# Kernel tuning notes

Measured on AMD Instinct MI355X. Metric: run time of the kernel, lower is better.

The kernel has to match this reference:

```python
import jax, jax.numpy as jnp
import numpy as np
import math

NUM_HEADS = 16


def setup_inputs() -> dict:
    key = jax.random.key(0)
    ks = jax.random.split(key, 7)
    B, S, D = 2, 2048, 1024
    scale = 1.0 / math.sqrt(D)
    return {
        "query": jax.random.normal(ks[0], (B, S, D), jnp.float32),
        "key": jax.random.normal(ks[1], (B, S, D), jnp.float32),
        "value": jax.random.normal(ks[2], (B, S, D), jnp.float32),
        "Wq": jax.random.normal(ks[3], (D, D), jnp.float32) * scale,
        "Wk": jax.random.normal(ks[4], (D, D), jnp.float32) * scale,
        "Wv": jax.random.normal(ks[5], (D, D), jnp.float32) * scale,
        "Wo": jax.random.normal(ks[6], (D, D), jnp.float32) * scale,
    }


def reference(query, key, value, Wq, Wk, Wv, Wo):
    B, Sq, D = query.shape
    Sk = key.shape[1]
    H = NUM_HEADS
    dk = D // H
    # torch Linear (no bias): y = x @ W.T
    q = (query @ Wq.T).reshape(B, Sq, H, dk).transpose(0, 2, 1, 3)  # [B,H,Sq,dk]
    k = (key @ Wk.T).reshape(B, Sk, H, dk).transpose(0, 2, 1, 3)
    v = (value @ Wv.T).reshape(B, Sk, H, dk).transpose(0, 2, 1, 3)
    scores = jnp.einsum("bhqd,bhkd->bhqk", q, k) / jnp.sqrt(jnp.float32(dk))
    causal = jnp.tril(jnp.ones((Sq, Sk), dtype=bool))  # mask_future=True
    scores = jnp.where(causal[None, None], scores, jnp.float32(-1e9))
    p = jax.nn.softmax(scores, axis=-1)
    x = jnp.einsum("bhqk,bhkd->bhqd", p, v)  # [B,H,Sq,dk]
    x = x.transpose(0, 2, 1, 3).reshape(B, Sq, D)
    return x @ Wo.T
```

## Files before the change

### kernel.cpp

```cpp
#include <hip/hip_runtime.h>
#include <hip/hip_bf16.h>
#include <stdint.h>

#define D_MODEL 1024
#define NHEADS  16
#define DK      64
#define SEQ     2048
#define BATCH   2

typedef __bf16 bf16x8 __attribute__((ext_vector_type(8)));
typedef __bf16 bf16x4 __attribute__((ext_vector_type(4)));
typedef float  f32x4  __attribute__((ext_vector_type(4)));

__device__ __forceinline__ void async_copy16(const void* g, void* l) {
  __builtin_amdgcn_global_load_lds(
      (__attribute__((address_space(1))) void*)g,
      (__attribute__((address_space(3))) void*)l, 16, 0, 0);
}

__global__ void cast_all(const float* __restrict__ q, const float* __restrict__ k,
                         const float* __restrict__ v, const float* __restrict__ wq,
                         const float* __restrict__ wk, const float* __restrict__ wv,
                         const float* __restrict__ wo,
                         __bf16* __restrict__ oq, __bf16* __restrict__ ok,
                         __bf16* __restrict__ ov, __bf16* __restrict__ owq,
                         __bf16* __restrict__ owk, __bf16* __restrict__ owv,
                         __bf16* __restrict__ owo) {
  constexpr unsigned Q4 = (unsigned)(BATCH * SEQ * D_MODEL) / 4;
  constexpr unsigned W4 = (unsigned)(D_MODEL * D_MODEL) / 4;
  unsigned i = blockIdx.x * 256u + threadIdx.x;
  const float* in; __bf16* out; unsigned off;
  if (i < 3 * Q4) {
    unsigned z = i >> 20; off = i & (Q4 - 1);
    in  = z == 0 ? q : z == 1 ? k : v;
    out = z == 0 ? oq : z == 1 ? ok : ov;
  } else {
    unsigned j = i - 3 * Q4;
    unsigned z = j >> 18; off = j & (W4 - 1);
    in  = z == 0 ? wq : z == 1 ? wk : z == 2 ? wv : wo;
    out = z == 0 ? owq : z == 1 ? owk : z == 2 ? owv : owo;
  }
  float4 val = *(const float4*)(in + (size_t)off * 4);
  bf16x4 o;
  o.x = (__bf16)val.x; o.y = (__bf16)val.y; o.z = (__bf16)val.z; o.w = (__bf16)val.w;
  *(bf16x4*)(out + (size_t)off * 4) = o;
}

template <int BM, int BN, typename OutT>
__global__ __launch_bounds__(256, 2)
void gemm_bt(const __bf16* __restrict__ A0, const __bf16* __restrict__ A1, const __bf16* __restrict__ A2,
             const __bf16* __restrict__ B0, const __bf16* __restrict__ B1, const __bf16* __restrict__ B2,
             OutT* __restrict__ C0, OutT* __restrict__ C1, OutT* __restrict__ C2,
             int M, int N, int K) {
  constexpr int MI = BM / 32, NJ = BN / 32;
  const __bf16* A; const __bf16* Bm; OutT* C;
  if (blockIdx.z == 0)      { A = A0; Bm = B0; C = C0; }
  else if (blockIdx.z == 1) { A = A1; Bm = B1; C = C1; }
  else                      { A = A2; Bm = B2; C = C2; }

  __shared__ __bf16 Ash[BM * 32];
  __shared__ __bf16 Bsh[BN * 32];

  const int tid  = threadIdx.x;
  const int lane = tid & 63;
  const int w    = tid >> 6;
  const int quad = lane >> 4;
  const int l16  = lane & 15;
  const int wr   = w >> 1, wc = w & 1;
  const size_t m0 = (size_t)blockIdx.x * BM;
  const size_t n0 = (size_t)blockIdx.y * BN;

  f32x4 acc[MI][NJ] = {};

  for (int k0 = 0; k0 < K; k0 += 32) {
#pragma unroll
    for (int it = 0; it < BM / 64; ++it) {
      int slot = tid + it * 256;
      async_copy16(A + (m0 + (slot >> 2)) * K + k0 + (slot & 3) * 8, &Ash[slot * 8]);
    }
#pragma unroll
    for (int it = 0; it < BN / 64; ++it) {
      int slot = tid + it * 256;
      async_copy16(Bm + (n0 + (slot >> 2)) * K + k0 + (slot & 3) * 8, &Bsh[slot * 8]);
    }
    __syncthreads();
    bf16x8 af[MI], bfr[NJ];
#pragma unroll
    for (int i = 0; i < MI; ++i)
      af[i] = *(const bf16x8*)&Ash[(wr * (BM / 2) + i * 16 + l16) * 32 + quad * 8];
#pragma unroll
    for (int j = 0; j < NJ; ++j)
      bfr[j] = *(const bf16x8*)&Bsh[(wc * (BN / 2) + j * 16 + l16) * 32 + quad * 8];
#pragma unroll
    for (int i = 0; i < MI; ++i)
#pragma unroll
      for (int j = 0; j < NJ; ++j)
        acc[i][j] = __builtin_amdgcn_mfma_f32_16x16x32_bf16(af[i], bfr[j], acc[i][j], 0, 0, 0);
    __syncthreads();
  }

#pragma unroll
  for (int i = 0; i < MI; ++i)
#pragma unroll
    for (int j = 0; j < NJ; ++j)
#pragma unroll
      for (int r = 0; r < 4; ++r) {
        size_t row = m0 + wr * (BM / 2) + i * 16 + quad * 4 + r;
        size_t col = n0 + wc * (BN / 2) + j * 16 + l16;
        C[row * N + col] = (OutT)acc[i][j][r];
      }
}

__global__ __launch_bounds__(256, 4)
void transpose_v(const __bf16* __restrict__ Vp, __bf16* __restrict__ Vt) {
  __shared__ __bf16 L[64 * 65];
  const int t  = threadIdx.x;
  const int s0 = blockIdx.x * 64, d0 = blockIdx.y * 64, b = blockIdx.z;
#pragma unroll
  for (int it = 0; it < 2; ++it) {
    int slot = t + it * 256;
    int sl = slot >> 3, c = slot & 7;
    int4 v = *(const int4*)&Vp[((size_t)(b * SEQ + s0 + sl)) * D_MODEL + d0 + c * 8];
    __bf16 tmp[8];
    *(int4*)tmp = v;
#pragma unroll
    for (int e = 0; e < 8; ++e) L[(c * 8 + e) * 65 + sl] = tmp[e];
  }
  __syncthreads();
#pragma unroll
  for (int it = 0; it < 2; ++it) {
    int slot = t + it * 256;
    int dl = slot >> 3, c2 = slot & 7;
    __bf16 tmp[8];
#pragma unroll
    for (int e = 0; e < 8; ++e) tmp[e] = L[dl * 65 + c2 * 8 + e];
    *(int4*)&Vt[((size_t)(b * D_MODEL + d0 + dl)) * SEQ + s0 + c2 * 8] = *(int4*)tmp;
  }
}

#define PS_W 40

__global__ __launch_bounds__(256, 3)
void attn_kernel(const __bf16* __restrict__ Qp, const __bf16* __restrict__ Kp,
                 const __bf16* __restrict__ Vt, __bf16* __restrict__ Xo) {
  __shared__ __bf16 Kb[2 * 2 * 64 * 32];
  __shared__ __bf16 Vb[2 * 2 * 64 * 32];
  __shared__ __bf16 Ps[4 * 32 * PS_W];
  __shared__ float  Xch[2 * 16 * 66];
  __shared__ float  Lsum[2 * 32];

  const int tid  = threadIdx.x;
  const int lane = tid & 63;
  const int w    = tid >> 6;
  const int qh   = w >> 1, kh = w & 1;
  const int quad = lane >> 4;
  const int l16  = lane & 15;
  const int bh   = blockIdx.x;
  const int pair = blockIdx.y;
  const int b    = bh >> 4, h = bh & 15;
  const size_t baseRow = (size_t)b * SEQ;
  const int colBase = h * DK;

  const int srow = w * 16 + (lane >> 2);
  const int sk   = (lane & 3) * 8;

  const float c1 = 0.18033688011f;
  const float c2 = -23.083120654f;

#pragma unroll 1
  for (int half = 0; half < 2; ++half) {
    const int qt = half == 0 ? (31 - pair) : pair;
    const int q0 = qt * 64;

    bf16x8 aq[2][2];
    {
      const __bf16* qrow = Qp + (baseRow + q0 + qh * 32 + l16) * D_MODEL + colBase;
#pragma unroll
      for (int mt = 0; mt < 2; ++mt)
#pragma unroll
        for (int kd = 0; kd < 2; ++kd)
          aq[mt][kd] = *(const bf16x8*)(qrow + (size_t)mt * 16 * D_MODEL + kd * 32 + quad * 8);
    }

    f32x4 oacc[2][4] = {};
    float plsum[2][4] = {};

    __syncthreads();
    {
      const __bf16* kbase = Kp + (baseRow + srow) * D_MODEL + colBase + sk;
      async_copy16(kbase,      &Kb[0 * 2048 + srow * 32 + sk]);
      async_copy16(kbase + 32, &Kb[1 * 2048 + srow * 32 + sk]);
      const __bf16* vbase = Vt + ((size_t)b * D_MODEL + colBase + srow) * SEQ + sk;
      async_copy16(vbase,      &Vb[0 * 2048 + srow * 32 + sk]);
      async_copy16(vbase + 32, &Vb[1 * 2048 + srow * 32 + sk]);
    }

    for (int j = 0; j <= qt; ++j) {
      const int bf = j & 1;
      __syncthreads();

      if (j < qt) {
        const int nb = bf ^ 1;
        const __bf16* kbase = Kp + (baseRow + (size_t)(j + 1) * 64 + srow) * D_MODEL + colBase + sk;
        async_copy16(kbase,      &Kb[(nb * 2 + 0) * 2048 + srow * 32 + sk]);
        async_copy16(kbase + 32, &Kb[(nb * 2 + 1) * 2048 + srow * 32 + sk]);
        const __bf16* vbase = Vt + ((size_t)b * D_MODEL + colBase + srow) * SEQ + (size_t)(j + 1) * 64 + sk;
        async_copy16(vbase,      &Vb[(nb * 2 + 0) * 2048 + srow * 32 + sk]);
        async_copy16(vbase + 32, &Vb[(nb * 2 + 1) * 2048 + srow * 32 + sk]);
      }

      f32x4 sacc[2][2] = {};
#pragma unroll
      for (int kd = 0; kd < 2; ++kd) {
        bf16x8 bk0 = *(const bf16x8*)&Kb[(bf * 2 + kd) * 2048 + (kh * 32 + l16) * 32 + quad * 8];
        bf16x8 bk1 = *(const bf16x8*)&Kb[(bf * 2 + kd) * 2048 + (kh * 32 + 16 + l16) * 32 + quad * 8];
        sacc[0][0] = __builtin_amdgcn_mfma_f32_16x16x32_bf16(aq[0][kd], bk0, sacc[0][0], 0, 0, 0);
        sacc[0][1] = __builtin_amdgcn_mfma_f32_16x16x32_bf16(aq[0][kd], bk1, sacc[0][1], 0, 0, 0);
        sacc[1][0] = __builtin_amdgcn_mfma_f32_16x16x32_bf16(aq[1][kd], bk0, sacc[1][0], 0, 0, 0);
        sacc[1][1] = __builtin_amdgcn_mfma_f32_16x16x32_bf16(aq[1][kd], bk1, sacc[1][1], 0, 0, 0);
      }

      const bool diag = (j == qt);
#pragma unroll
      for (int mt = 0; mt < 2; ++mt)
#pragma unroll
        for (int nt2 = 0; nt2 < 2; ++nt2)
#pragma unroll
          for (int r = 0; r < 4; ++r) {
            float arg = fmaf(sacc[mt][nt2][r], c1, c2);
            if (diag) {
              int rowg = q0 + qh * 32 + mt * 16 + quad * 4 + r;
              int colg = j * 64 + kh * 32 + nt2 * 16 + l16;
              if (colg > rowg) arg = -1e30f;
            }
            float p = __builtin_amdgcn_exp2f(arg);
            plsum[mt][r] += p;
            Ps[(w * 32 + mt * 16 + quad * 4 + r) * PS_W + nt2 * 16 + l16] = (__bf16)p;
          }

      bf16x8 bv[4];
#pragma unroll
      for (int nt = 0; nt < 4; ++nt)
        bv[nt] = *(const bf16x8*)&Vb[(bf * 2 + kh) * 2048 + (nt * 16 + l16) * 32 + quad * 8];
#pragma unroll
      for (int mt = 0; mt < 2; ++mt) {
        bf16x8 ap = *(const bf16x8*)&Ps[(w * 32 + mt * 16 + l16) * PS_W + quad * 8];
#pragma unroll
        for (int nt = 0; nt < 4; ++nt)
          oacc[mt][nt] = __builtin_amdgcn_mfma_f32_16x16x32_bf16(ap, bv[nt], oacc[mt][nt], 0, 0, 0);
      }
    }

    float lred[2][4];
#pragma unroll
    for (int mt = 0; mt < 2; ++mt)
#pragma unroll
      for (int r = 0; r < 4; ++r) {
        float l = plsum[mt][r];
        for (int off = 1; off < 16; off <<= 1) l += __shfl_xor(l, off, 64);
        lred[mt][r] = l;
      }

#pragma unroll
    for (int mt = 0; mt < 2; ++mt) {
      __syncthreads();
      if (kh == 1) {
#pragma unroll
        for (int nt = 0; nt < 4; ++nt)
#pragma unroll
          for (int r = 0; r < 4; ++r)
            Xch[(qh * 16 + quad * 4 + r) * 66 + nt * 16 + l16] = oacc[mt][nt][r];
#pragma unroll
        for (int r = 0; r < 4; ++r)
          Lsum[qh * 32 + mt * 16 + quad * 4 + r] = lred[mt][r];
      }
      __syncthreads();
      if (kh == 0) {
#pragma unroll
        for (int r = 0; r < 4; ++r) {
          float lt  = lred[mt][r] + Lsum[qh * 32 + mt * 16 + quad * 4 + r];
          float inv = 1.0f / lt;
          size_t row = baseRow + q0 + qh * 32 + mt * 16 + quad * 4 + r;
#pragma unroll
          for (int nt = 0; nt < 4; ++nt) {
            float o = oacc[mt][nt][r] + Xch[(qh * 16 + quad * 4 + r) * 66 + nt * 16 + l16];
            Xo[row * D_MODEL + colBase + nt * 16 + l16] = (__bf16)(o * inv);
          }
        }
      }
    }
  }
}

extern "C" void kernel_launch(void* const* d_in, const int* in_sizes, int n_in,
                              void* d_out, int out_size, void* d_ws, size_t ws_size,
                              hipStream_t stream) {
  const float* q  = (const float*)d_in[0];
  const float* k  = (const float*)d_in[1];
  const float* v  = (const float*)d_in[2];
  const float* wq = (const float*)d_in[3];
  const float* wk = (const float*)d_in[4];
  const float* wv = (const float*)d_in[5];
  const float* wo = (const float*)d_in[6];
  float* out = (float*)d_out;

  const size_t MD = (size_t)BATCH * SEQ * D_MODEL;
  const size_t WD = (size_t)D_MODEL * D_MODEL;
  __bf16* ws  = (__bf16*)d_ws;
  __bf16* Qp  = ws;
  __bf16* Kp  = Qp + MD;
  __bf16* Vp  = Kp + MD;
  __bf16* Xa  = Vp + MD;
  __bf16* qbf = Xa + MD;
  __bf16* kbf = qbf + MD;
  __bf16* vbf = kbf + MD;
  __bf16* wqb = vbf + MD;
  __bf16* wkb = wqb + WD;
  __bf16* wvb = wkb + WD;
  __bf16* wob = wvb + WD;
  __bf16* Vt  = qbf;

  cast_all<<<16384, 256, 0, stream>>>(q, k, v, wq, wk, wv, wo,
                                      qbf, kbf, vbf, wqb, wkb, wvb, wob);

  gemm_bt<128, 128, __bf16><<<dim3(32, 8, 3), 256, 0, stream>>>(
      qbf, kbf, vbf, wqb, wkb, wvb, Qp, Kp, Vp,
      BATCH * SEQ, D_MODEL, D_MODEL);

  transpose_v<<<dim3(SEQ / 64, D_MODEL / 64, BATCH), 256, 0, stream>>>(Vp, Vt);

  attn_kernel<<<dim3(BATCH * NHEADS, 16), 256, 0, stream>>>(Qp, Kp, Vt, Xa);

  gemm_bt<64, 128, float><<<dim3(64, 8, 1), 256, 0, stream>>>(
      Xa, Xa, Xa, wob, wob, wob, out, out, out,
      BATCH * SEQ, D_MODEL, D_MODEL);
}
```

Before: 209.2 us.

## Fuse fp32-to-bf16 activation cast into QKV GEMM and unpair attention tiles

The QKV projection GEMM now loads fp32 activations straight into LDS with a swizzled layout and converts them to bf16 in registers. This removes the separate cast pass over the three large input tensors and its bf16 intermediate buffers, leaving only a small cast kernel for the weights. The attention kernel also stops pairing a long and a short causal query tile per block and launches one block per query tile instead (32 per head). That doubles the grid but gives blocks uneven amounts of work. The fp32 A tile doubles LDS traffic and LDS footprint in the GEMM.

```diff
diff --git a/kernel.cpp b/kernel.cpp
--- a/kernel.cpp
+++ b/kernel.cpp
@@ -18,46 +18,98 @@
       (__attribute__((address_space(3))) void*)l, 16, 0, 0);
 }
 
-__global__ void cast_all(const float* __restrict__ q, const float* __restrict__ k,
-                         const float* __restrict__ v, const float* __restrict__ wq,
-                         const float* __restrict__ wk, const float* __restrict__ wv,
-                         const float* __restrict__ wo,
-                         __bf16* __restrict__ oq, __bf16* __restrict__ ok,
-                         __bf16* __restrict__ ov, __bf16* __restrict__ owq,
-                         __bf16* __restrict__ owk, __bf16* __restrict__ owv,
-                         __bf16* __restrict__ owo) {
-  constexpr unsigned Q4 = (unsigned)(BATCH * SEQ * D_MODEL) / 4;
-  constexpr unsigned W4 = (unsigned)(D_MODEL * D_MODEL) / 4;
-  unsigned i = blockIdx.x * 256u + threadIdx.x;
-  const float* in; __bf16* out; unsigned off;
-  if (i < 3 * Q4) {
-    unsigned z = i >> 20; off = i & (Q4 - 1);
-    in  = z == 0 ? q : z == 1 ? k : v;
-    out = z == 0 ? oq : z == 1 ? ok : ov;
-  } else {
-    unsigned j = i - 3 * Q4;
-    unsigned z = j >> 18; off = j & (W4 - 1);
-    in  = z == 0 ? wq : z == 1 ? wk : z == 2 ? wv : wo;
-    out = z == 0 ? owq : z == 1 ? owk : z == 2 ? owv : owo;
-  }
-  float4 val = *(const float4*)(in + (size_t)off * 4);
+__global__ void cast_w(const float* __restrict__ wq, const float* __restrict__ wk,
+                       const float* __restrict__ wv, const float* __restrict__ wo,
+                       __bf16* __restrict__ owq, __bf16* __restrict__ owk,
+                       __bf16* __restrict__ owv, __bf16* __restrict__ owo) {
+  const float* in = blockIdx.y == 0 ? wq : blockIdx.y == 1 ? wk : blockIdx.y == 2 ? wv : wo;
+  __bf16* out     = blockIdx.y == 0 ? owq : blockIdx.y == 1 ? owk : blockIdx.y == 2 ? owv : owo;
+  size_t i = (size_t)(blockIdx.x * 256 + threadIdx.x) * 4;
+  float4 val = *(const float4*)(in + i);
   bf16x4 o;
   o.x = (__bf16)val.x; o.y = (__bf16)val.y; o.z = (__bf16)val.z; o.w = (__bf16)val.w;
-  *(bf16x4*)(out + (size_t)off * 4) = o;
-}
-
-template <int BM, int BN, typename OutT>
+  *(bf16x4*)(out + i) = o;
+}
+
 __global__ __launch_bounds__(256, 2)
-void gemm_bt(const __bf16* __restrict__ A0, const __bf16* __restrict__ A1, const __bf16* __restrict__ A2,
-             const __bf16* __restrict__ B0, const __bf16* __restrict__ B1, const __bf16* __restrict__ B2,
-             OutT* __restrict__ C0, OutT* __restrict__ C1, OutT* __restrict__ C2,
-             int M, int N, int K) {
-  constexpr int MI = BM / 32, NJ = BN / 32;
-  const __bf16* A; const __bf16* Bm; OutT* C;
+void gemm_af32_bt(const float* __restrict__ A0, const float* __restrict__ A1, const float* __restrict__ A2,
+                  const __bf16* __restrict__ B0, const __bf16* __restrict__ B1, const __bf16* __restrict__ B2,
+                  __bf16* __restrict__ C0, __bf16* __restrict__ C1, __bf16* __restrict__ C2,
+                  int M, int N, int K) {
+  const float* A; const __bf16* Bm; __bf16* C;
   if (blockIdx.z == 0)      { A = A0; Bm = B0; C = C0; }
   else if (blockIdx.z == 1) { A = A1; Bm = B1; C = C1; }
   else                      { A = A2; Bm = B2; C = C2; }
 
+  __shared__ float  Ashf[128 * 32];
+  __shared__ __bf16 Bsh[128 * 32];
+
+  const int tid  = threadIdx.x;
+  const int lane = tid & 63;
+  const int w    = tid >> 6;
+  const int quad = lane >> 4;
+  const int l16  = lane & 15;
+  const int wr   = w >> 1, wc = w & 1;
+  const size_t m0 = (size_t)blockIdx.x * 128;
+  const size_t n0 = (size_t)blockIdx.y * 128;
+
+  f32x4 acc[4][4] = {};
+
+  for (int k0 = 0; k0 < K; k0 += 32) {
+#pragma unroll
+    for (int it = 0; it < 4; ++it) {
+      int slot = tid + it * 256;
+      int row = slot >> 3, pos = slot & 7;
+      int cc  = pos ^ (row & 7);
+      async_copy16(A + (m0 + row) * K + k0 + cc * 4, &Ashf[slot * 4]);
+    }
+#pragma unroll
+    for (int it = 0; it < 2; ++it) {
+      int slot = tid + it * 256;
+      async_copy16(Bm + (n0 + (slot >> 2)) * K + k0 + (slot & 3) * 8, &Bsh[slot * 8]);
+    }
+    __syncthreads();
+
+    bf16x8 af[4], bfr[4];
+#pragma unroll
+    for (int i = 0; i < 4; ++i) {
+      int row = wr * 64 + i * 16 + l16;
+      int p0 = (2 * quad) ^ (row & 7);
+      f32x4 lo = *(const f32x4*)&Ashf[row * 32 + p0 * 4];
+      f32x4 hi = *(const f32x4*)&Ashf[row * 32 + (p0 ^ 1) * 4];
+      bf16x8 t;
+      t[0] = (__bf16)lo[0]; t[1] = (__bf16)lo[1]; t[2] = (__bf16)lo[2]; t[3] = (__bf16)lo[3];
+      t[4] = (__bf16)hi[0]; t[5] = (__bf16)hi[1]; t[6] = (__bf16)hi[2]; t[7] = (__bf16)hi[3];
+      af[i] = t;
+    }
+#pragma unroll
+    for (int j = 0; j < 4; ++j)
+      bfr[j] = *(const bf16x8*)&Bsh[(wc * 64 + j * 16 + l16) * 32 + quad * 8];
+#pragma unroll
+    for (int i = 0; i < 4; ++i)
+#pragma unroll
+      for (int j = 0; j < 4; ++j)
+        acc[i][j] = __builtin_amdgcn_mfma_f32_16x16x32_bf16(af[i], bfr[j], acc[i][j], 0, 0, 0);
+    __syncthreads();
+  }
+
+#pragma unroll
+  for (int i = 0; i < 4; ++i)
+#pragma unroll
+    for (int j = 0; j < 4; ++j)
+#pragma unroll
+      for (int r = 0; r < 4; ++r) {
+        size_t row = m0 + wr * 64 + i * 16 + quad * 4 + r;
+        size_t col = n0 + wc * 64 + j * 16 + l16;
+        C[row * N + col] = (__bf16)acc[i][j][r];
+      }
+}
+
+template <int BM, int BN, typename OutT>
+__global__ __launch_bounds__(256, 2)
+void gemm_bt(const __bf16* __restrict__ A, const __bf16* __restrict__ Bm,
+             OutT* __restrict__ C, int M, int N, int K) {
+  constexpr int MI = BM / 32, NJ = BN / 32;
   __shared__ __bf16 Ash[BM * 32];
   __shared__ __bf16 Bsh[BN * 32];
 
@@ -156,8 +208,9 @@
   const int quad = lane >> 4;
   const int l16  = lane & 15;
   const int bh   = blockIdx.x;
-  const int pair = blockIdx.y;
+  const int qt   = 31 - blockIdx.y;
   const int b    = bh >> 4, h = bh & 15;
+  const int q0   = qt * 64;
   const size_t baseRow = (size_t)b * SEQ;
   const int colBase = h * DK;
 
@@ -167,125 +220,118 @@
   const float c1 = 0.18033688011f;
   const float c2 = -23.083120654f;
 
-#pragma unroll 1
-  for (int half = 0; half < 2; ++half) {
-    const int qt = half == 0 ? (31 - pair) : pair;
-    const int q0 = qt * 64;
-
-    bf16x8 aq[2][2];
-    {
-      const __bf16* qrow = Qp + (baseRow + q0 + qh * 32 + l16) * D_MODEL + colBase;
-#pragma unroll
-      for (int mt = 0; mt < 2; ++mt)
-#pragma unroll
-        for (int kd = 0; kd < 2; ++kd)
-          aq[mt][kd] = *(const bf16x8*)(qrow + (size_t)mt * 16 * D_MODEL + kd * 32 + quad * 8);
-    }
-
-    f32x4 oacc[2][4] = {};
-    float plsum[2][4] = {};
-
-    __syncthreads();
-    {
-      const __bf16* kbase = Kp + (baseRow + srow) * D_MODEL + colBase + sk;
-      async_copy16(kbase,      &Kb[0 * 2048 + srow * 32 + sk]);
-      async_copy16(kbase + 32, &Kb[1 * 2048 + srow * 32 + sk]);
-      const __bf16* vbase = Vt + ((size_t)b * D_MODEL + colBase + srow) * SEQ + sk;
-      async_copy16(vbase,      &Vb[0 * 2048 + srow * 32 + sk]);
-      async_copy16(vbase + 32, &Vb[1 * 2048 + srow * 32 + sk]);
-    }
-
-    for (int j = 0; j <= qt; ++j) {
-      const int bf = j & 1;
-      __syncthreads();
-
-      if (j < qt) {
-        const int nb = bf ^ 1;
-        const __bf16* kbase = Kp + (baseRow + (size_t)(j + 1) * 64 + srow) * D_MODEL + colBase + sk;
-        async_copy16(kbase,      &Kb[(nb * 2 + 0) * 2048 + srow * 32 + sk]);
-        async_copy16(kbase + 32, &Kb[(nb * 2 + 1) * 2048 + srow * 32 + sk]);
-        const __bf16* vbase = Vt + ((size_t)b * D_MODEL + colBase + srow) * SEQ + (size_t)(j + 1) * 64 + sk;
-        async_copy16(vbase,      &Vb[(nb * 2 + 0) * 2048 + srow * 32 + sk]);
-        async_copy16(vbase + 32, &Vb[(nb * 2 + 1) * 2048 + srow * 32 + sk]);
-      }
-
-      f32x4 sacc[2][2] = {};
-#pragma unroll
-      for (int kd = 0; kd < 2; ++kd) {
-        bf16x8 bk0 = *(const bf16x8*)&Kb[(bf * 2 + kd) * 2048 + (kh * 32 + l16) * 32 + quad * 8];
-        bf16x8 bk1 = *(const bf16x8*)&Kb[(bf * 2 + kd) * 2048 + (kh * 32 + 16 + l16) * 32 + quad * 8];
-        sacc[0][0] = __builtin_amdgcn_mfma_f32_16x16x32_bf16(aq[0][kd], bk0, sacc[0][0], 0, 0, 0);
-        sacc[0][1] = __builtin_amdgcn_mfma_f32_16x16x32_bf16(aq[0][kd], bk1, sacc[0][1], 0, 0, 0);
-        sacc[1][0] = __builtin_amdgcn_mfma_f32_16x16x32_bf16(aq[1][kd], bk0, sacc[1][0], 0, 0, 0);
-        sacc[1][1] = __builtin_amdgcn_mfma_f32_16x16x32_bf16(aq[1][kd], bk1, sacc[1][1], 0, 0, 0);
-      }
-
-      const bool diag = (j == qt);
-#pragma unroll
-      for (int mt = 0; mt < 2; ++mt)
-#pragma unroll
-        for (int nt2 = 0; nt2 < 2; ++nt2)
-#pragma unroll
-          for (int r = 0; r < 4; ++r) {
-            float arg = fmaf(sacc[mt][nt2][r], c1, c2);
-            if (diag) {
-              int rowg = q0 + qh * 32 + mt * 16 + quad * 4 + r;
-              int colg = j * 64 + kh * 32 + nt2 * 16 + l16;
-              if (colg > rowg) arg = -1e30f;
-            }
-            float p = __builtin_amdgcn_exp2f(arg);
-            plsum[mt][r] += p;
-            Ps[(w * 32 + mt * 16 + quad * 4 + r) * PS_W + nt2 * 16 + l16] = (__bf16)p;
+  bf16x8 aq[2][2];
+  {
+    const __bf16* qrow = Qp + (baseRow + q0 + qh * 32 + l16) * D_MODEL + colBase;
+#pragma unroll
+    for (int mt = 0; mt < 2; ++mt)
+#pragma unroll
+      for (int kd = 0; kd < 2; ++kd)
+        aq[mt][kd] = *(const bf16x8*)(qrow + (size_t)mt * 16 * D_MODEL + kd * 32 + quad * 8);
+  }
+
+  f32x4 oacc[2][4] = {};
+  float plsum[2][4] = {};
+
+  {
+    const __bf16* kbase = Kp + (baseRow + srow) * D_MODEL + colBase + sk;
+    async_copy16(kbase,      &Kb[0 * 2048 + srow * 32 + sk]);
+    async_copy16(kbase + 32, &Kb[1 * 2048 + srow * 32 + sk]);
+    const __bf16* vbase = Vt + ((size_t)b * D_MODEL + colBase + srow) * SEQ + sk;
+    async_copy16(vbase,      &Vb[0 * 2048 + srow * 32 + sk]);
+    async_copy16(vbase + 32, &Vb[1 * 2048 + srow * 32 + sk]);
+  }
+
+  for (int j = 0; j <= qt; ++j) {
+    const int bf = j & 1;
+    __syncthreads();
+
+    if (j < qt) {
+      const int nb = bf ^ 1;
+      const __bf16* kbase = Kp + (baseRow + (size_t)(j + 1) * 64 + srow) * D_MODEL + colBase + sk;
+      async_copy16(kbase,      &Kb[(nb * 2 + 0) * 2048 + srow * 32 + sk]);
+      async_copy16(kbase + 32, &Kb[(nb * 2 + 1) * 2048 + srow * 32 + sk]);
+      const __bf16* vbase = Vt + ((size_t)b * D_MODEL + colBase + srow) * SEQ + (size_t)(j + 1) * 64 + sk;
+      async_copy16(vbase,      &Vb[(nb * 2 + 0) * 2048 + srow * 32 + sk]);
+      async_copy16(vbase + 32, &Vb[(nb * 2 + 1) * 2048 + srow * 32 + sk]);
+    }
+
+    f32x4 sacc[2][2] = {};
+#pragma unroll
+    for (int kd = 0; kd < 2; ++kd) {
+      bf16x8 bk0 = *(const bf16x8*)&Kb[(bf * 2 + kd) * 2048 + (kh * 32 + l16) * 32 + quad * 8];
+      bf16x8 bk1 = *(const bf16x8*)&Kb[(bf * 2 + kd) * 2048 + (kh * 32 + 16 + l16) * 32 + quad * 8];
+      sacc[0][0] = __builtin_amdgcn_mfma_f32_16x16x32_bf16(aq[0][kd], bk0, sacc[0][0], 0, 0, 0);
+      sacc[0][1] = __builtin_amdgcn_mfma_f32_16x16x32_bf16(aq[0][kd], bk1, sacc[0][1], 0, 0, 0);
+      sacc[1][0] = __builtin_amdgcn_mfma_f32_16x16x32_bf16(aq[1][kd], bk0, sacc[1][0], 0, 0, 0);
+      sacc[1][1] = __builtin_amdgcn_mfma_f32_16x16x32_bf16(aq[1][kd], bk1, sacc[1][1], 0, 0, 0);
+    }
+
+    const bool diag = (j == qt);
+#pragma unroll
+    for (int mt = 0; mt < 2; ++mt)
+#pragma unroll
+      for (int nt2 = 0; nt2 < 2; ++nt2)
+#pragma unroll
+        for (int r = 0; r < 4; ++r) {
+          float arg = fmaf(sacc[mt][nt2][r], c1, c2);
+          if (diag) {
+            int rowg = q0 + qh * 32 + mt * 16 + quad * 4 + r;
+            int colg = j * 64 + kh * 32 + nt2 * 16 + l16;
+            if (colg > rowg) arg = -1e30f;
           }
-
-      bf16x8 bv[4];
+          float p = __builtin_amdgcn_exp2f(arg);
+          plsum[mt][r] += p;
+          Ps[(w * 32 + mt * 16 + quad * 4 + r) * PS_W + nt2 * 16 + l16] = (__bf16)p;
+        }
+
+    bf16x8 bv[4];
+#pragma unroll
+    for (int nt = 0; nt < 4; ++nt)
+      bv[nt] = *(const bf16x8*)&Vb[(bf * 2 + kh) * 2048 + (nt * 16 + l16) * 32 + quad * 8];
+#pragma unroll
+    for (int mt = 0; mt < 2; ++mt) {
+      bf16x8 ap = *(const bf16x8*)&Ps[(w * 32 + mt * 16 + l16) * PS_W + quad * 8];
 #pragma unroll
       for (int nt = 0; nt < 4; ++nt)
-        bv[nt] = *(const bf16x8*)&Vb[(bf * 2 + kh) * 2048 + (nt * 16 + l16) * 32 + quad * 8];
-#pragma unroll
-      for (int mt = 0; mt < 2; ++mt) {
-        bf16x8 ap = *(const bf16x8*)&Ps[(w * 32 + mt * 16 + l16) * PS_W + quad * 8];
-#pragma unroll
-        for (int nt = 0; nt < 4; ++nt)
-          oacc[mt][nt] = __builtin_amdgcn_mfma_f32_16x16x32_bf16(ap, bv[nt], oacc[mt][nt], 0, 0, 0);
-      }
-    }
-
-    float lred[2][4];
-#pragma unroll
-    for (int mt = 0; mt < 2; ++mt)
+        oacc[mt][nt] = __builtin_amdgcn_mfma_f32_16x16x32_bf16(ap, bv[nt], oacc[mt][nt], 0, 0, 0);
+    }
+  }
+
+  float lred[2][4];
+#pragma unroll
+  for (int mt = 0; mt < 2; ++mt)
+#pragma unroll
+    for (int r = 0; r < 4; ++r) {
+      float l = plsum[mt][r];
+      for (int off = 1; off < 16; off <<= 1) l += __shfl_xor(l, off, 64);
+      lred[mt][r] = l;
+    }
+
+#pragma unroll
+  for (int mt = 0; mt < 2; ++mt) {
+    __syncthreads();
+    if (kh == 1) {
+#pragma unroll
+      for (int nt = 0; nt < 4; ++nt)
+#pragma unroll
+        for (int r = 0; r < 4; ++r)
+          Xch[(qh * 16 + quad * 4 + r) * 66 + nt * 16 + l16] = oacc[mt][nt][r];
+#pragma unroll
+      for (int r = 0; r < 4; ++r)
+        Lsum[qh * 32 + mt * 16 + quad * 4 + r] = lred[mt][r];
+    }
+    __syncthreads();
+    if (kh == 0) {
 #pragma unroll
       for (int r = 0; r < 4; ++r) {
-        float l = plsum[mt][r];
-        for (int off = 1; off < 16; off <<= 1) l += __shfl_xor(l, off, 64);
-        lred[mt][r] = l;
-      }
-
-#pragma unroll
-    for (int mt = 0; mt < 2; ++mt) {
-      __syncthreads();
-      if (kh == 1) {
-#pragma unroll
-        for (int nt = 0; nt < 4; ++nt)
-#pragma unroll
-          for (int r = 0; r < 4; ++r)
-            Xch[(qh * 16 + quad * 4 + r) * 66 + nt * 16 + l16] = oacc[mt][nt][r];
-#pragma unroll
-        for (int r = 0; r < 4; ++r)
-          Lsum[qh * 32 + mt * 16 + quad * 4 + r] = lred[mt][r];
-      }
-      __syncthreads();
-      if (kh == 0) {
-#pragma unroll
-        for (int r = 0; r < 4; ++r) {
-          float lt  = lred[mt][r] + Lsum[qh * 32 + mt * 16 + quad * 4 + r];
-          float inv = 1.0f / lt;
-          size_t row = baseRow + q0 + qh * 32 + mt * 16 + quad * 4 + r;
-#pragma unroll
-          for (int nt = 0; nt < 4; ++nt) {
-            float o = oacc[mt][nt][r] + Xch[(qh * 16 + quad * 4 + r) * 66 + nt * 16 + l16];
-            Xo[row * D_MODEL + colBase + nt * 16 + l16] = (__bf16)(o * inv);
-          }
+        float lt  = lred[mt][r] + Lsum[qh * 32 + mt * 16 + quad * 4 + r];
+        float inv = 1.0f / lt;
+        size_t row = baseRow + q0 + qh * 32 + mt * 16 + quad * 4 + r;
+#pragma unroll
+        for (int nt = 0; nt < 4; ++nt) {
+          float o = oacc[mt][nt][r] + Xch[(qh * 16 + quad * 4 + r) * 66 + nt * 16 + l16];
+          Xo[row * D_MODEL + colBase + nt * 16 + l16] = (__bf16)(o * inv);
         }
       }
     }
@@ -311,27 +357,22 @@
   __bf16* Kp  = Qp + MD;
   __bf16* Vp  = Kp + MD;
   __bf16* Xa  = Vp + MD;
-  __bf16* qbf = Xa + MD;
-  __bf16* kbf = qbf + MD;
-  __bf16* vbf = kbf + MD;
-  __bf16* wqb = vbf + MD;
+  __bf16* Vt  = Xa + MD;
+  __bf16* wqb = Vt + MD;
   __bf16* wkb = wqb + WD;
   __bf16* wvb = wkb + WD;
   __bf16* wob = wvb + WD;
-  __bf16* Vt  = qbf;
-
-  cast_all<<<16384, 256, 0, stream>>>(q, k, v, wq, wk, wv, wo,
-                                      qbf, kbf, vbf, wqb, wkb, wvb, wob);
-
-  gemm_bt<128, 128, __bf16><<<dim3(32, 8, 3), 256, 0, stream>>>(
-      qbf, kbf, vbf, wqb, wkb, wvb, Qp, Kp, Vp,
+
+  cast_w<<<dim3((int)(WD / 1024), 4), 256, 0, stream>>>(wq, wk, wv, wo, wqb, wkb, wvb, wob);
+
+  gemm_af32_bt<<<dim3(32, 8, 3), 256, 0, stream>>>(
+      q, k, v, wqb, wkb, wvb, Qp, Kp, Vp,
       BATCH * SEQ, D_MODEL, D_MODEL);
 
   transpose_v<<<dim3(SEQ / 64, D_MODEL / 64, BATCH), 256, 0, stream>>>(Vp, Vt);
 
-  attn_kernel<<<dim3(BATCH * NHEADS, 16), 256, 0, stream>>>(Qp, Kp, Vt, Xa);
-
-  gemm_bt<64, 128, float><<<dim3(64, 8, 1), 256, 0, stream>>>(
-      Xa, Xa, Xa, wob, wob, wob, out, out, out,
-      BATCH * SEQ, D_MODEL, D_MODEL);
-}
+  attn_kernel<<<dim3(BATCH * NHEADS, 32), 256, 0, stream>>>(Qp, Kp, Vt, Xa);
+
+  gemm_bt<64, 128, float><<<dim3(64, 8), 256, 0, stream>>>(
+      Xa, wob, out, BATCH * SEQ, D_MODEL, D_MODEL);
+}
```

Measured after the change: 225.0 us. 1.08x slower.

## Fuse V transpose into projection GEMM and split attention query tiles per block

Applied to the files above, without the earlier changes.

The projection GEMM now writes V transposed straight from an LDS staging tile, which removes the separate transpose kernel and its extra global round trip. The attention kernel no longer pairs a long and a short query tile in one block. It launches one block per query tile (32 per head) and orders them so the heaviest tiles are dispatched first. The GEMMs are specialised to compile-time sizes. The projection kernel uses a large extra LDS buffer and launch bounds of 3, which may limit occupancy, and the unpaired attention blocks could load-balance worse.

```diff
diff --git a/kernel.cpp b/kernel.cpp
--- a/kernel.cpp
+++ b/kernel.cpp
@@ -46,18 +46,97 @@
   *(bf16x4*)(out + (size_t)off * 4) = o;
 }
 
-template <int BM, int BN, typename OutT>
+__global__ __launch_bounds__(256, 3)
+void gemm_proj(const __bf16* __restrict__ A0, const __bf16* __restrict__ A1, const __bf16* __restrict__ A2,
+               const __bf16* __restrict__ B0, const __bf16* __restrict__ B1, const __bf16* __restrict__ B2,
+               __bf16* __restrict__ Qp, __bf16* __restrict__ Kp, __bf16* __restrict__ Vt) {
+  constexpr int K = D_MODEL, N = D_MODEL;
+  const int zi = blockIdx.z;
+  const __bf16* A; const __bf16* Bm;
+  if (zi == 0)      { A = A0; Bm = B0; }
+  else if (zi == 1) { A = A1; Bm = B1; }
+  else              { A = A2; Bm = B2; }
+
+  __shared__ __bf16 Ash[128 * 32];
+  __shared__ __bf16 Bsh[128 * 32];
+  __shared__ __align__(16) __bf16 Tr[128 * 136];
+
+  const int tid  = threadIdx.x;
+  const int lane = tid & 63;
+  const int w    = tid >> 6;
+  const int quad = lane >> 4;
+  const int l16  = lane & 15;
+  const int wr   = w >> 1, wc = w & 1;
+  const size_t m0 = (size_t)blockIdx.x * 128;
+  const size_t n0 = (size_t)blockIdx.y * 128;
+
+  f32x4 acc[4][4] = {};
+
+  for (int k0 = 0; k0 < K; k0 += 32) {
+#pragma unroll
+    for (int it = 0; it < 2; ++it) {
+      int slot = tid + it * 256;
+      async_copy16(A + (m0 + (slot >> 2)) * K + k0 + (slot & 3) * 8, &Ash[slot * 8]);
+    }
+#pragma unroll
+    for (int it = 0; it < 2; ++it) {
+      int slot = tid + it * 256;
+      async_copy16(Bm + (n0 + (slot >> 2)) * K + k0 + (slot & 3) * 8, &Bsh[slot * 8]);
+    }
+    __syncthreads();
+    bf16x8 af[4], bfr[4];
+#pragma unroll
+    for (int i = 0; i < 4; ++i)
+      af[i] = *(const bf16x8*)&Ash[(wr * 64 + i * 16 + l16) * 32 + quad * 8];
+#pragma unroll
+    for (int j = 0; j < 4; ++j)
+      bfr[j] = *(const bf16x8*)&Bsh[(wc * 64 + j * 16 + l16) * 32 + quad * 8];
+#pragma unroll
+    for (int i = 0; i < 4; ++i)
+#pragma unroll
+      for (int j = 0; j < 4; ++j)
+        acc[i][j] = __builtin_amdgcn_mfma_f32_16x16x32_bf16(af[i], bfr[j], acc[i][j], 0, 0, 0);
+    __syncthreads();
+  }
+
+  if (zi != 2) {
+    __bf16* C = (zi == 0) ? Qp : Kp;
+#pragma unroll
+    for (int i = 0; i < 4; ++i)
+#pragma unroll
+      for (int j = 0; j < 4; ++j)
+#pragma unroll
+        for (int r = 0; r < 4; ++r) {
+          size_t row = m0 + wr * 64 + i * 16 + quad * 4 + r;
+          size_t col = n0 + wc * 64 + j * 16 + l16;
+          C[row * N + col] = (__bf16)acc[i][j][r];
+        }
+  } else {
+#pragma unroll
+    for (int i = 0; i < 4; ++i)
+#pragma unroll
+      for (int j = 0; j < 4; ++j)
+#pragma unroll
+        for (int r = 0; r < 4; ++r)
+          Tr[(wc * 64 + j * 16 + l16) * 136 + (wr * 64 + i * 16 + quad * 4 + r)] =
+              (__bf16)acc[i][j][r];
+    __syncthreads();
+    const int b_  = (int)(m0 >> 11);
+    const int sl0 = (int)(m0 & 2047);
+#pragma unroll
+    for (int it = 0; it < 8; ++it) {
+      int slot = tid + it * 256;
+      int d = slot >> 4, sc = slot & 15;
+      *(int4*)&Vt[((size_t)(b_ * D_MODEL) + n0 + d) * SEQ + sl0 + sc * 8] =
+          *(const int4*)&Tr[d * 136 + sc * 8];
+    }
+  }
+}
+
 __global__ __launch_bounds__(256, 2)
-void gemm_bt(const __bf16* __restrict__ A0, const __bf16* __restrict__ A1, const __bf16* __restrict__ A2,
-             const __bf16* __restrict__ B0, const __bf16* __restrict__ B1, const __bf16* __restrict__ B2,
-             OutT* __restrict__ C0, OutT* __restrict__ C1, OutT* __restrict__ C2,
-             int M, int N, int K) {
-  constexpr int MI = BM / 32, NJ = BN / 32;
-  const __bf16* A; const __bf16* Bm; OutT* C;
-  if (blockIdx.z == 0)      { A = A0; Bm = B0; C = C0; }
-  else if (blockIdx.z == 1) { A = A1; Bm = B1; C = C1; }
-  else                      { A = A2; Bm = B2; C = C2; }
-
+void gemm_out(const __bf16* __restrict__ A, const __bf16* __restrict__ Bm,
+              float* __restrict__ C) {
+  constexpr int BM = 64, BN = 128, K = D_MODEL, N = D_MODEL;
   __shared__ __bf16 Ash[BM * 32];
   __shared__ __bf16 Bsh[BN * 32];
 
@@ -70,72 +149,44 @@
   const size_t m0 = (size_t)blockIdx.x * BM;
   const size_t n0 = (size_t)blockIdx.y * BN;
 
-  f32x4 acc[MI][NJ] = {};
+  f32x4 acc[2][4] = {};
 
   for (int k0 = 0; k0 < K; k0 += 32) {
-#pragma unroll
-    for (int it = 0; it < BM / 64; ++it) {
-      int slot = tid + it * 256;
+    {
+      int slot = tid;
       async_copy16(A + (m0 + (slot >> 2)) * K + k0 + (slot & 3) * 8, &Ash[slot * 8]);
     }
 #pragma unroll
-    for (int it = 0; it < BN / 64; ++it) {
+    for (int it = 0; it < 2; ++it) {
       int slot = tid + it * 256;
       async_copy16(Bm + (n0 + (slot >> 2)) * K + k0 + (slot & 3) * 8, &Bsh[slot * 8]);
     }
     __syncthreads();
-    bf16x8 af[MI], bfr[NJ];
-#pragma unroll
-    for (int i = 0; i < MI; ++i)
-      af[i] = *(const bf16x8*)&Ash[(wr * (BM / 2) + i * 16 + l16) * 32 + quad * 8];
-#pragma unroll
-    for (int j = 0; j < NJ; ++j)
-      bfr[j] = *(const bf16x8*)&Bsh[(wc * (BN / 2) + j * 16 + l16) * 32 + quad * 8];
-#pragma unroll
-    for (int i = 0; i < MI; ++i)
-#pragma unroll
-      for (int j = 0; j < NJ; ++j)
+    bf16x8 af[2], bfr[4];
+#pragma unroll
+    for (int i = 0; i < 2; ++i)
+      af[i] = *(const bf16x8*)&Ash[(wr * 32 + i * 16 + l16) * 32 + quad * 8];
+#pragma unroll
+    for (int j = 0; j < 4; ++j)
+      bfr[j] = *(const bf16x8*)&Bsh[(wc * 64 + j * 16 + l16) * 32 + quad * 8];
+#pragma unroll
+    for (int i = 0; i < 2; ++i)
+#pragma unroll
+      for (int j = 0; j < 4; ++j)
         acc[i][j] = __builtin_amdgcn_mfma_f32_16x16x32_bf16(af[i], bfr[j], acc[i][j], 0, 0, 0);
     __syncthreads();
   }
 
 #pragma unroll
-  for (int i = 0; i < MI; ++i)
-#pragma unroll
-    for (int j = 0; j < NJ; ++j)
+  for (int i = 0; i < 2; ++i)
+#pragma unroll
+    for (int j = 0; j < 4; ++j)
 #pragma unroll
       for (int r = 0; r < 4; ++r) {
-        size_t row = m0 + wr * (BM / 2) + i * 16 + quad * 4 + r;
-        size_t col = n0 + wc * (BN / 2) + j * 16 + l16;
-        C[row * N + col] = (OutT)acc[i][j][r];
+        size_t row = m0 + wr * 32 + i * 16 + quad * 4 + r;
+        size_t col = n0 + wc * 64 + j * 16 + l16;
+        C[row * N + col] = acc[i][j][r];
       }
-}
-
-__global__ __launch_bounds__(256, 4)
-void transpose_v(const __bf16* __restrict__ Vp, __bf16* __restrict__ Vt) {
-  __shared__ __bf16 L[64 * 65];
-  const int t  = threadIdx.x;
-  const int s0 = blockIdx.x * 64, d0 = blockIdx.y * 64, b = blockIdx.z;
-#pragma unroll
-  for (int it = 0; it < 2; ++it) {
-    int slot = t + it * 256;
-    int sl = slot >> 3, c = slot & 7;
-    int4 v = *(const int4*)&Vp[((size_t)(b * SEQ + s0 + sl)) * D_MODEL + d0 + c * 8];
-    __bf16 tmp[8];
-    *(int4*)tmp = v;
-#pragma unroll
-    for (int e = 0; e < 8; ++e) L[(c * 8 + e) * 65 + sl] = tmp[e];
-  }
-  __syncthreads();
-#pragma unroll
-  for (int it = 0; it < 2; ++it) {
-    int slot = t + it * 256;
-    int dl = slot >> 3, c2 = slot & 7;
-    __bf16 tmp[8];
-#pragma unroll
-    for (int e = 0; e < 8; ++e) tmp[e] = L[dl * 65 + c2 * 8 + e];
-    *(int4*)&Vt[((size_t)(b * D_MODEL + d0 + dl)) * SEQ + s0 + c2 * 8] = *(int4*)tmp;
-  }
 }
 
 #define PS_W 40
@@ -156,8 +207,9 @@
   const int quad = lane >> 4;
   const int l16  = lane & 15;
   const int bh   = blockIdx.x;
-  const int pair = blockIdx.y;
+  const int qt   = 31 - blockIdx.y;
   const int b    = bh >> 4, h = bh & 15;
+  const int q0   = qt * 64;
   const size_t baseRow = (size_t)b * SEQ;
   const int colBase = h * DK;
 
@@ -167,125 +219,118 @@
   const float c1 = 0.18033688011f;
   const float c2 = -23.083120654f;
 
-#pragma unroll 1
-  for (int half = 0; half < 2; ++half) {
-    const int qt = half == 0 ? (31 - pair) : pair;
-    const int q0 = qt * 64;
-
-    bf16x8 aq[2][2];
-    {
-      const __bf16* qrow = Qp + (baseRow + q0 + qh * 32 + l16) * D_MODEL + colBase;
-#pragma unroll
-      for (int mt = 0; mt < 2; ++mt)
-#pragma unroll
-        for (int kd = 0; kd < 2; ++kd)
-          aq[mt][kd] = *(const bf16x8*)(qrow + (size_t)mt * 16 * D_MODEL + kd * 32 + quad * 8);
-    }
-
-    f32x4 oacc[2][4] = {};
-    float plsum[2][4] = {};
-
-    __syncthreads();
-    {
-      const __bf16* kbase = Kp + (baseRow + srow) * D_MODEL + colBase + sk;
-      async_copy16(kbase,      &Kb[0 * 2048 + srow * 32 + sk]);
-      async_copy16(kbase + 32, &Kb[1 * 2048 + srow * 32 + sk]);
-      const __bf16* vbase = Vt + ((size_t)b * D_MODEL + colBase + srow) * SEQ + sk;
-      async_copy16(vbase,      &Vb[0 * 2048 + srow * 32 + sk]);
-      async_copy16(vbase + 32, &Vb[1 * 2048 + srow * 32 + sk]);
-    }
-
-    for (int j = 0; j <= qt; ++j) {
-      const int bf = j & 1;
-      __syncthreads();
-
-      if (j < qt) {
-        const int nb = bf ^ 1;
-        const __bf16* kbase = Kp + (baseRow + (size_t)(j + 1) * 64 + srow) * D_MODEL + colBase + sk;
-        async_copy16(kbase,      &Kb[(nb * 2 + 0) * 2048 + srow * 32 + sk]);
-        async_copy16(kbase + 32, &Kb[(nb * 2 + 1) * 2048 + srow * 32 + sk]);
-        const __bf16* vbase = Vt + ((size_t)b * D_MODEL + colBase + srow) * SEQ + (size_t)(j + 1) * 64 + sk;
-        async_copy16(vbase,      &Vb[(nb * 2 + 0) * 2048 + srow * 32 + sk]);
-        async_copy16(vbase + 32, &Vb[(nb * 2 + 1) * 2048 + srow * 32 + sk]);
-      }
-
-      f32x4 sacc[2][2] = {};
-#pragma unroll
-      for (int kd = 0; kd < 2; ++kd) {
-        bf16x8 bk0 = *(const bf16x8*)&Kb[(bf * 2 + kd) * 2048 + (kh * 32 + l16) * 32 + quad * 8];
-        bf16x8 bk1 = *(const bf16x8*)&Kb[(bf * 2 + kd) * 2048 + (kh * 32 + 16 + l16) * 32 + quad * 8];
-        sacc[0][0] = __builtin_amdgcn_mfma_f32_16x16x32_bf16(aq[0][kd], bk0, sacc[0][0], 0, 0, 0);
-        sacc[0][1] = __builtin_amdgcn_mfma_f32_16x16x32_bf16(aq[0][kd], bk1, sacc[0][1], 0, 0, 0);
-        sacc[1][0] = __builtin_amdgcn_mfma_f32_16x16x32_bf16(aq[1][kd], bk0, sacc[1][0], 0, 0, 0);
-        sacc[1][1] = __builtin_amdgcn_mfma_f32_16x16x32_bf16(aq[1][kd], bk1, sacc[1][1], 0, 0, 0);
-      }
-
-      const bool diag = (j == qt);
-#pragma unroll
-      for (int mt = 0; mt < 2; ++mt)
-#pragma unroll
-        for (int nt2 = 0; nt2 < 2; ++nt2)
-#pragma unroll
-          for (int r = 0; r < 4; ++r) {
-            float arg = fmaf(sacc[mt][nt2][r], c1, c2);
-            if (diag) {
-              int rowg = q0 + qh * 32 + mt * 16 + quad * 4 + r;
-              int colg = j * 64 + kh * 32 + nt2 * 16 + l16;
-              if (colg > rowg) arg = -1e30f;
-            }
-            float p = __builtin_amdgcn_exp2f(arg);
-            plsum[mt][r] += p;
-            Ps[(w * 32 + mt * 16 + quad * 4 + r) * PS_W + nt2 * 16 + l16] = (__bf16)p;
+  bf16x8 aq[2][2];
+  {
+    const __bf16* qrow = Qp + (baseRow + q0 + qh * 32 + l16) * D_MODEL + colBase;
+#pragma unroll
+    for (int mt = 0; mt < 2; ++mt)
+#pragma unroll
+      for (int kd = 0; kd < 2; ++kd)
+        aq[mt][kd] = *(const bf16x8*)(qrow + (size_t)mt * 16 * D_MODEL + kd * 32 + quad * 8);
+  }
+
+  f32x4 oacc[2][4] = {};
+  float plsum[2][4] = {};
+
+  {
+    const __bf16* kbase = Kp + (baseRow + srow) * D_MODEL + colBase + sk;
+    async_copy16(kbase,      &Kb[0 * 2048 + srow * 32 + sk]);
+    async_copy16(kbase + 32, &Kb[1 * 2048 + srow * 32 + sk]);
+    const __bf16* vbase = Vt + ((size_t)b * D_MODEL + colBase + srow) * SEQ + sk;
+    async_copy16(vbase,      &Vb[0 * 2048 + srow * 32 + sk]);
+    async_copy16(vbase + 32, &Vb[1 * 2048 + srow * 32 + sk]);
+  }
+
+  for (int j = 0; j <= qt; ++j) {
+    const int bf = j & 1;
+    __syncthreads();
+
+    if (j < qt) {
+      const int nb = bf ^ 1;
+      const __bf16* kbase = Kp + (baseRow + (size_t)(j + 1) * 64 + srow) * D_MODEL + colBase + sk;
+      async_copy16(kbase,      &Kb[(nb * 2 + 0) * 2048 + srow * 32 + sk]);
+      async_copy16(kbase + 32, &Kb[(nb * 2 + 1) * 2048 + srow * 32 + sk]);
+      const __bf16* vbase = Vt + ((size_t)b * D_MODEL + colBase + srow) * SEQ + (size_t)(j + 1) * 64 + sk;
+      async_copy16(vbase,      &Vb[(nb * 2 + 0) * 2048 + srow * 32 + sk]);
+      async_copy16(vbase + 32, &Vb[(nb * 2 + 1) * 2048 + srow * 32 + sk]);
+    }
+
+    f32x4 sacc[2][2] = {};
+#pragma unroll
+    for (int kd = 0; kd < 2; ++kd) {
+      bf16x8 bk0 = *(const bf16x8*)&Kb[(bf * 2 + kd) * 2048 + (kh * 32 + l16) * 32 + quad * 8];
+      bf16x8 bk1 = *(const bf16x8*)&Kb[(bf * 2 + kd) * 2048 + (kh * 32 + 16 + l16) * 32 + quad * 8];
+      sacc[0][0] = __builtin_amdgcn_mfma_f32_16x16x32_bf16(aq[0][kd], bk0, sacc[0][0], 0, 0, 0);
+      sacc[0][1] = __builtin_amdgcn_mfma_f32_16x16x32_bf16(aq[0][kd], bk1, sacc[0][1], 0, 0, 0);
+      sacc[1][0] = __builtin_amdgcn_mfma_f32_16x16x32_bf16(aq[1][kd], bk0, sacc[1][0], 0, 0, 0);
+      sacc[1][1] = __builtin_amdgcn_mfma_f32_16x16x32_bf16(aq[1][kd], bk1, sacc[1][1], 0, 0, 0);
+    }
+
+    const bool diag = (j == qt);
+#pragma unroll
+    for (int mt = 0; mt < 2; ++mt)
+#pragma unroll
+      for (int nt2 = 0; nt2 < 2; ++nt2)
+#pragma unroll
+        for (int r = 0; r < 4; ++r) {
+          float arg = fmaf(sacc[mt][nt2][r], c1, c2);
+          if (diag) {
+            int rowg = q0 + qh * 32 + mt * 16 + quad * 4 + r;
+            int colg = j * 64 + kh * 32 + nt2 * 16 + l16;
+            if (colg > rowg) arg = -1e30f;
           }
-
-      bf16x8 bv[4];
+          float p = __builtin_amdgcn_exp2f(arg);
+          plsum[mt][r] += p;
+          Ps[(w * 32 + mt * 16 + quad * 4 + r) * PS_W + nt2 * 16 + l16] = (__bf16)p;
+        }
+
+    bf16x8 bv[4];
+#pragma unroll
+    for (int nt = 0; nt < 4; ++nt)
+      bv[nt] = *(const bf16x8*)&Vb[(bf * 2 + kh) * 2048 + (nt * 16 + l16) * 32 + quad * 8];
+#pragma unroll
+    for (int mt = 0; mt < 2; ++mt) {
+      bf16x8 ap = *(const bf16x8*)&Ps[(w * 32 + mt * 16 + l16) * PS_W + quad * 8];
 #pragma unroll
       for (int nt = 0; nt < 4; ++nt)
-        bv[nt] = *(const bf16x8*)&Vb[(bf * 2 + kh) * 2048 + (nt * 16 + l16) * 32 + quad * 8];
-#pragma unroll
-      for (int mt = 0; mt < 2; ++mt) {
-        bf16x8 ap = *(const bf16x8*)&Ps[(w * 32 + mt * 16 + l16) * PS_W + quad * 8];
-#pragma unroll
-        for (int nt = 0; nt < 4; ++nt)
-          oacc[mt][nt] = __builtin_amdgcn_mfma_f32_16x16x32_bf16(ap, bv[nt], oacc[mt][nt], 0, 0, 0);
-      }
-    }
-
-    float lred[2][4];
-#pragma unroll
-    for (int mt = 0; mt < 2; ++mt)
+        oacc[mt][nt] = __builtin_amdgcn_mfma_f32_16x16x32_bf16(ap, bv[nt], oacc[mt][nt], 0, 0, 0);
+    }
+  }
+
+  float lred[2][4];
+#pragma unroll
+  for (int mt = 0; mt < 2; ++mt)
+#pragma unroll
+    for (int r = 0; r < 4; ++r) {
+      float l = plsum[mt][r];
+      for (int off = 1; off < 16; off <<= 1) l += __shfl_xor(l, off, 64);
+      lred[mt][r] = l;
+    }
+
+#pragma unroll
+  for (int mt = 0; mt < 2; ++mt) {
+    __syncthreads();
+    if (kh == 1) {
+#pragma unroll
+      for (int nt = 0; nt < 4; ++nt)
+#pragma unroll
+        for (int r = 0; r < 4; ++r)
+          Xch[(qh * 16 + quad * 4 + r) * 66 + nt * 16 + l16] = oacc[mt][nt][r];
+#pragma unroll
+      for (int r = 0; r < 4; ++r)
+        Lsum[qh * 32 + mt * 16 + quad * 4 + r] = lred[mt][r];
+    }
+    __syncthreads();
+    if (kh == 0) {
 #pragma unroll
       for (int r = 0; r < 4; ++r) {
-        float l = plsum[mt][r];
-        for (int off = 1; off < 16; off <<= 1) l += __shfl_xor(l, off, 64);
-        lred[mt][r] = l;
-      }
-
-#pragma unroll
-    for (int mt = 0; mt < 2; ++mt) {
-      __syncthreads();
-      if (kh == 1) {
-#pragma unroll
-        for (int nt = 0; nt < 4; ++nt)
-#pragma unroll
-          for (int r = 0; r < 4; ++r)
-            Xch[(qh * 16 + quad * 4 + r) * 66 + nt * 16 + l16] = oacc[mt][nt][r];
-#pragma unroll
-        for (int r = 0; r < 4; ++r)
-          Lsum[qh * 32 + mt * 16 + quad * 4 + r] = lred[mt][r];
-      }
-      __syncthreads();
-      if (kh == 0) {
-#pragma unroll
-        for (int r = 0; r < 4; ++r) {
-          float lt  = lred[mt][r] + Lsum[qh * 32 + mt * 16 + quad * 4 + r];
-          float inv = 1.0f / lt;
-          size_t row = baseRow + q0 + qh * 32 + mt * 16 + quad * 4 + r;
-#pragma unroll
-          for (int nt = 0; nt < 4; ++nt) {
-            float o = oacc[mt][nt][r] + Xch[(qh * 16 + quad * 4 + r) * 66 + nt * 16 + l16];
-            Xo[row * D_MODEL + colBase + nt * 16 + l16] = (__bf16)(o * inv);
-          }
+        float lt  = lred[mt][r] + Lsum[qh * 32 + mt * 16 + quad * 4 + r];
+        float inv = 1.0f / lt;
+        size_t row = baseRow + q0 + qh * 32 + mt * 16 + quad * 4 + r;
+#pragma unroll
+        for (int nt = 0; nt < 4; ++nt) {
+          float o = oacc[mt][nt][r] + Xch[(qh * 16 + quad * 4 + r) * 66 + nt * 16 + l16];
+          Xo[row * D_MODEL + colBase + nt * 16 + l16] = (__bf16)(o * inv);
         }
       }
     }
@@ -309,8 +354,8 @@
   __bf16* ws  = (__bf16*)d_ws;
   __bf16* Qp  = ws;
   __bf16* Kp  = Qp + MD;
-  __bf16* Vp  = Kp + MD;
-  __bf16* Xa  = Vp + MD;
+  __bf16* Vt  = Kp + MD;
+  __bf16* Xa  = Vt + MD;
   __bf16* qbf = Xa + MD;
   __bf16* kbf = qbf + MD;
   __bf16* vbf = kbf + MD;
@@ -318,20 +363,14 @@
   __bf16* wkb = wqb + WD;
   __bf16* wvb = wkb + WD;
   __bf16* wob = wvb + WD;
-  __bf16* Vt  = qbf;
 
   cast_all<<<16384, 256, 0, stream>>>(q, k, v, wq, wk, wv, wo,
                                       qbf, kbf, vbf, wqb, wkb, wvb, wob);
 
-  gemm_bt<128, 128, __bf16><<<dim3(32, 8, 3), 256, 0, stream>>>(
-      qbf, kbf, vbf, wqb, wkb, wvb, Qp, Kp, Vp,
-      BATCH * SEQ, D_MODEL, D_MODEL);
-
-  transpose_v<<<dim3(SEQ / 64, D_MODEL / 64, BATCH), 256, 0, stream>>>(Vp, Vt);
-
-  attn_kernel<<<dim3(BATCH * NHEADS, 16), 256, 0, stream>>>(Qp, Kp, Vt, Xa);
-
-  gemm_bt<64, 128, float><<<dim3(64, 8, 1), 256, 0, stream>>>(
-      Xa, Xa, Xa, wob, wob, wob, out, out, out,
-      BATCH * SEQ, D_MODEL, D_MODEL);
-}
+  gemm_proj<<<dim3(32, 8, 3), 256, 0, stream>>>(
+      qbf, kbf, vbf, wqb, wkb, wvb, Qp, Kp, Vt);
+
+  attn_kernel<<<dim3(BATCH * NHEADS, 32), 256, 0, stream>>>(Qp, Kp, Vt, Xa);
+
+  gemm_out<<<dim3(64, 8), 256, 0, stream>>>(Xa, wob, out);
+}
```

After: 200.4 us. -4.2%, faster.
